# Kernel optimization log

Hardware: AMD Instinct MI355X
Metric: run time of the kernel (lower is better)

The kernel has to match this reference:

```python
import jax, jax.numpy as jnp
import numpy as np
import math

NUM_HEADS = 16
KEY_DIM = 64
MODEL_DIM = 1024
NEG_INF = -1000000000.0


def _get_slopes(n):
    def pow2_slopes(n):
        start = 2 ** (-2 ** (-(math.log2(n) - 3)))
        return [start * start ** i for i in range(n)]
    if math.log2(n).is_integer():
        s = pow2_slopes(n)
    else:
        c = 2 ** math.floor(math.log2(n))
        s = pow2_slopes(c) + pow2_slopes(2 * c)[0::2][: n - c]
    return jnp.asarray(s, dtype=jnp.float32)


def setup_inputs() -> dict:
    key = jax.random.key(0)
    ks = jax.random.split(key, 11)
    B, S, D = 4, 2048, MODEL_DIM
    P = NUM_HEADS * KEY_DIM
    sd = 1.0 / math.sqrt(D)
    return {
        "query": jax.random.normal(ks[0], (B, S, D), jnp.float32),
        "key": jax.random.normal(ks[1], (B, S, D), jnp.float32),
        "value": jax.random.normal(ks[2], (B, S, D), jnp.float32),
        "Wq": jax.random.normal(ks[3], (D, P), jnp.float32) * sd,
        "bq": jnp.zeros((P,), jnp.float32),
        "Wk": jax.random.normal(ks[4], (D, P), jnp.float32) * sd,
        "bk": jnp.zeros((P,), jnp.float32),
        "Wv": jax.random.normal(ks[5], (D, P), jnp.float32) * sd,
        "bv": jnp.zeros((P,), jnp.float32),
        "Wo": jax.random.normal(ks[6], (P, D), jnp.float32) * (1.0 / math.sqrt(P)),
        "bo": jnp.zeros((D,), jnp.float32),
    }


def reference(query, key, value, Wq, bq, Wk, bk, Wv, bv, Wo, bo):
    B, S, _ = query.shape
    H, Kd = NUM_HEADS, KEY_DIM

    def split_heads(x):  # [B,S,H*Kd] -> [B,H,S,Kd]
        return x.reshape(B, S, H, Kd).transpose(0, 2, 1, 3)

    q = split_heads(query @ Wq + bq)
    k = split_heads(key @ Wk + bk)
    v = split_heads(value @ Wv + bv)

    logits = jnp.einsum("bhqd,bhkd->bhqk", q, k) / jnp.sqrt(jnp.float32(Kd))

    i = jnp.arange(S)[:, None]
    j = jnp.arange(S)[None, :]
    causal = jnp.where(i >= j, 0.0, NEG_INF).astype(jnp.float32)  # [S,S]
    rel = (i - j).astype(jnp.float32)  # [S,S]
    slopes = _get_slopes(H)  # [H]
    alibi = slopes[:, None, None] * rel  # [H,S,S]
    logits = logits + causal[None, None, :, :] + alibi[None, :, :, :]

    weights = jax.nn.softmax(logits, axis=-1)
    attn = jnp.einsum("bhqk,bhkd->bhqd", weights, v)
    concat = attn.transpose(0, 2, 1, 3).reshape(B, S, H * Kd)
    return concat @ Wo + bo
```

## Files before the change

### kernel.cpp

```cpp
#include <hip/hip_runtime.h>

#define B_ 4
#define S_ 2048
#define D_ 1024
#define H_ 16
#define KD_ 64
#define P_ 1024
#define M_ (B_*S_)

typedef unsigned short u16;
typedef unsigned int u32;
typedef __attribute__((ext_vector_type(2))) unsigned u32x2;
typedef __attribute__((ext_vector_type(4))) float f32x4;
typedef __attribute__((ext_vector_type(8))) __bf16 bf16x8;

__device__ __forceinline__ u16 f2bf(float f) {
  u32 x = __float_as_uint(f);
  return (u16)((x + 0x7fffu + ((x >> 16) & 1u)) >> 16);
}

__device__ __forceinline__ void gl_lds16(const u16* g, u16* l) {
  __builtin_amdgcn_global_load_lds((__attribute__((address_space(1))) void*)g,
                                   (__attribute__((address_space(3))) void*)l, 16, 0, 0);
}

__device__ __forceinline__ u32 pkbf(float a, float b) {
  return __builtin_amdgcn_perm(__float_as_uint(b) + 0x8000u,
                               __float_as_uint(a) + 0x8000u, 0x07060302u);
}

#if __has_builtin(__builtin_amdgcn_permlane32_swap) && __has_builtin(__builtin_amdgcn_permlane16_swap)
__device__ __forceinline__ void plswap(u32& a, u32& b) {
  u32x2 r32 = __builtin_amdgcn_permlane32_swap(a, b, false, false);
  u32x2 r16 = __builtin_amdgcn_permlane16_swap(r32[0], r32[1], false, false);
  a = r16[0]; b = r16[1];
}
#else
__device__ __forceinline__ void plswap(u32& a, u32& b) {
  const int l = threadIdx.x & 63;
  const int quad = l >> 4, l16 = l & 15;
  int i0 = (((quad & 1) * 32) + l16) * 4;
  int i1 = i0 + 64;
  int a_lo = __builtin_amdgcn_ds_bpermute(i0, (int)a);
  int b_lo = __builtin_amdgcn_ds_bpermute(i0, (int)b);
  int a_hi = __builtin_amdgcn_ds_bpermute(i1, (int)a);
  int b_hi = __builtin_amdgcn_ds_bpermute(i1, (int)b);
  u32 na = (quad < 2) ? (u32)a_lo : (u32)b_lo;
  u32 nb = (quad < 2) ? (u32)a_hi : (u32)b_hi;
  a = na; b = nb;
}
#endif

__global__ void cvt3_kernel(const float* __restrict__ q, const float* __restrict__ k,
                            const float* __restrict__ v,
                            u16* __restrict__ Xq, u16* __restrict__ Xk, u16* __restrict__ Xv) {
  const int z = blockIdx.y;
  const float* in = z == 0 ? q : z == 1 ? k : v;
  u16* out = z == 0 ? Xq : z == 1 ? Xk : Xv;
  int i = blockIdx.x * 256 + threadIdx.x;
  float4 vv = ((const float4*)in)[i];
  ((u32*)out)[i*2+0] = (u32)f2bf(vv.x) | ((u32)f2bf(vv.y) << 16);
  ((u32*)out)[i*2+1] = (u32)f2bf(vv.z) | ((u32)f2bf(vv.w) << 16);
}

__global__ void transpose_cvt4(const float* __restrict__ Wq, const float* __restrict__ Wk,
                               const float* __restrict__ Wv, const float* __restrict__ Wo,
                               u16* __restrict__ WqT, u16* __restrict__ WkT,
                               u16* __restrict__ WvT, u16* __restrict__ WoT) {
  const int z = blockIdx.z;
  const float* in = z == 0 ? Wq : z == 1 ? Wk : z == 2 ? Wv : Wo;
  u16* out = z == 0 ? WqT : z == 1 ? WkT : z == 2 ? WvT : WoT;
  __shared__ float tile[32][33];
  int bx = blockIdx.x * 32, by = blockIdx.y * 32;
  int tx = threadIdx.x, ty = threadIdx.y;
  #pragma unroll
  for (int kk = 0; kk < 4; ++kk)
    tile[ty + kk*8][tx] = in[(by + ty + kk*8) * 1024 + bx + tx];
  __syncthreads();
  #pragma unroll
  for (int kk = 0; kk < 4; ++kk)
    out[(bx + ty + kk*8) * 1024 + by + tx] = f2bf(tile[tx][ty + kk*8]);
}

__global__ __launch_bounds__(256) void gemm_qkv(
    const u16* __restrict__ Xq, const u16* __restrict__ Xk, const u16* __restrict__ Xv,
    const u16* __restrict__ WqT, const u16* __restrict__ WkT, const u16* __restrict__ WvT,
    const float* __restrict__ bq, const float* __restrict__ bk, const float* __restrict__ bv,
    u16* __restrict__ Qb, u16* __restrict__ Kb, u16* __restrict__ Vt)
{
  constexpr int K = 1024, N = 1024, BK = 32;
  const int z = blockIdx.z;
  const u16* A  = z == 0 ? Xq  : z == 1 ? Xk  : Xv;
  const u16* Bt = z == 0 ? WqT : z == 1 ? WkT : WvT;
  const float* bias = z == 0 ? bq : z == 1 ? bk : bv;

  __shared__ alignas(16) u16 As[128*BK];
  __shared__ alignas(16) u16 Bs[128*BK];
  const int tid = threadIdx.x;
  const int w = tid >> 6, l = tid & 63;
  const int quad = l >> 4, l16 = l & 15;
  const int wm = (w >> 1) * 64, wn = (w & 1) * 64;
  const long mBase = (long)blockIdx.x * 128;
  const int  nBase = blockIdx.y * 128;

  f32x4 acc[4][4] = {};
  const int off0 = w*1024 + l*16;

  for (int kb = 0; kb < K/BK; ++kb) {
    __syncthreads();
    #pragma unroll
    for (int p = 0; p < 2; ++p) {
      int off = p*4096 + off0;
      int row = off >> 6;
      int cb  = off & 63;
      const u16* ga = A  + (mBase + row)*K + kb*BK + (cb >> 1);
      const u16* gb = Bt + ((long)(nBase + row))*K + kb*BK + (cb >> 1);
      gl_lds16(ga, (u16*)((char*)As + p*4096 + w*1024));
      gl_lds16(gb, (u16*)((char*)Bs + p*4096 + w*1024));
    }
    __syncthreads();
    bf16x8 af[4], bf[4];
    #pragma unroll
    for (int i = 0; i < 4; ++i) af[i] = *(const bf16x8*)&As[(wm + i*16 + l16)*BK + quad*8];
    #pragma unroll
    for (int j = 0; j < 4; ++j) bf[j] = *(const bf16x8*)&Bs[(wn + j*16 + l16)*BK + quad*8];
    #pragma unroll
    for (int i = 0; i < 4; ++i)
      #pragma unroll
      for (int j = 0; j < 4; ++j)
        acc[i][j] = __builtin_amdgcn_mfma_f32_16x16x32_bf16(af[i], bf[j], acc[i][j], 0, 0, 0);
  }

  if (z < 2) {
    u16* Cout = z == 0 ? Qb : Kb;
    #pragma unroll
    for (int i = 0; i < 4; ++i)
      #pragma unroll
      for (int j = 0; j < 4; ++j)
        #pragma unroll
        for (int r = 0; r < 4; ++r) {
          long row = mBase + wm + i*16 + quad*4 + r;
          int  col = nBase + wn + j*16 + l16;
          Cout[row*N + col] = f2bf(acc[i][j][r] + bias[col]);
        }
  } else {
    #pragma unroll
    for (int i = 0; i < 4; ++i)
      #pragma unroll
      for (int j = 0; j < 4; ++j) {
        int  col  = nBase + wn + j*16 + l16;
        long row0 = mBase + wm + i*16 + quad*4;
        int  bb = (int)(row0 >> 11);
        int  ss = (int)(row0 & 2047);
        float bcol = bias[col];
        float v0 = acc[i][j][0] + bcol, v1 = acc[i][j][1] + bcol;
        float v2 = acc[i][j][2] + bcol, v3 = acc[i][j][3] + bcol;
        uint2 pk;
        pk.x = (u32)f2bf(v0) | ((u32)f2bf(v1) << 16);
        pk.y = (u32)f2bf(v2) | ((u32)f2bf(v3) << 16);
        *(uint2*)&Vt[((long)(bb*16) * 64 + col) * 2048 + ss] = pk;
      }
  }
}

__global__ __launch_bounds__(256) void gemm_out(const u16* __restrict__ A,
                                                const u16* __restrict__ Bt,
                                                const float* __restrict__ bias,
                                                float* __restrict__ Cout)
{
  constexpr int K = 1024, N = 1024, BK = 32;
  __shared__ alignas(16) u16 As[128*BK];
  __shared__ alignas(16) u16 Bs[128*BK];
  const int tid = threadIdx.x;
  const int w = tid >> 6, l = tid & 63;
  const int quad = l >> 4, l16 = l & 15;
  const int wm = (w >> 1) * 64, wn = (w & 1) * 64;
  const long mBase = (long)blockIdx.x * 128;
  const int  nBase = blockIdx.y * 128;

  f32x4 acc[4][4] = {};
  const int off0 = w*1024 + l*16;

  for (int kb = 0; kb < K/BK; ++kb) {
    __syncthreads();
    #pragma unroll
    for (int p = 0; p < 2; ++p) {
      int off = p*4096 + off0;
      int row = off >> 6;
      int cb  = off & 63;
      const u16* ga = A  + (mBase + row)*K + kb*BK + (cb >> 1);
      const u16* gb = Bt + ((long)(nBase + row))*K + kb*BK + (cb >> 1);
      gl_lds16(ga, (u16*)((char*)As + p*4096 + w*1024));
      gl_lds16(gb, (u16*)((char*)Bs + p*4096 + w*1024));
    }
    __syncthreads();
    bf16x8 af[4], bf[4];
    #pragma unroll
    for (int i = 0; i < 4; ++i) af[i] = *(const bf16x8*)&As[(wm + i*16 + l16)*BK + quad*8];
    #pragma unroll
    for (int j = 0; j < 4; ++j) bf[j] = *(const bf16x8*)&Bs[(wn + j*16 + l16)*BK + quad*8];
    #pragma unroll
    for (int i = 0; i < 4; ++i)
      #pragma unroll
      for (int j = 0; j < 4; ++j)
        acc[i][j] = __builtin_amdgcn_mfma_f32_16x16x32_bf16(af[i], bf[j], acc[i][j], 0, 0, 0);
  }

  #pragma unroll
  for (int i = 0; i < 4; ++i)
    #pragma unroll
    for (int j = 0; j < 4; ++j)
      #pragma unroll
      for (int r = 0; r < 4; ++r) {
        long row = mBase + wm + i*16 + quad*4 + r;
        int  col = nBase + wn + j*16 + l16;
        Cout[row*N + col] = acc[i][j][r] + bias[col];
      }
}

__global__ __launch_bounds__(256, 4) void attn_kernel(const u16* __restrict__ Qb,
                                                      const u16* __restrict__ Kb,
                                                      const u16* __restrict__ Vt,
                                                      u16* __restrict__ Ob)
{
  const int n = blockIdx.x;
  const int qt = 15 - (n >> 6);
  const int r6 = n & 63;
  const int b = r6 >> 4, h = r6 & 15;
  const int w = threadIdx.x >> 6;
  const int l = threadIdx.x & 63;
  const int quad = l >> 4, l16 = l & 15;
  const float LOG2E = 1.44269504089f;
  const float slope = exp2f(-0.5f * (float)(h + 1));
  const float c1  = 0.125f * LOG2E;
  const float sl2 = slope * LOG2E;
  const float rs1 = sl2, rs2 = 2.f*sl2, rs3 = 3.f*sl2;

  const int q0 = qt*128 + w*32;
  const u16* Qp = Qb + ((long)(b*S_ + q0))*P_ + h*KD_;
  const u16* Kp = Kb + ((long)(b*S_))*P_ + h*KD_;
  const u16* Vp = Vt + ((long)(b*H_ + h))*KD_*S_;

  bf16x8 qf[2][2];
  #pragma unroll
  for (int i = 0; i < 2; ++i)
    #pragma unroll
    for (int kk = 0; kk < 2; ++kk)
      qf[i][kk] = *(const bf16x8*)&Qp[(long)(i*16 + l16)*P_ + kk*32 + quad*8];

  f32x4 o[2][4] = {};
  float lsum[2] = {0.f, 0.f};

  for (int kt = 0; kt < qt; ++kt) {
    const u16* kts = Kp + (long)(kt*128 + l16)*P_;
    const float kbase = (float)(kt*128);
    #pragma unroll
    for (int ks = 0; ks < 4; ++ks) {
      u32 pw[2][2][2];
      #pragma unroll
      for (int jp = 0; jp < 2; ++jp) {
        const int j = 2*ks + jp;
        const u16* kp = kts + (long)(j*16)*P_;
        bf16x8 kf0 = *(const bf16x8*)(kp + quad*8);
        bf16x8 kf1 = *(const bf16x8*)(kp + 32 + quad*8);
        const float bij = -sl2 * (kbase + (float)(j*16 + quad*4));
        #pragma unroll
        for (int i = 0; i < 2; ++i) {
          f32x4 t = {};
          t = __builtin_amdgcn_mfma_f32_16x16x32_bf16(kf0, qf[i][0], t, 0, 0, 0);
          t = __builtin_amdgcn_mfma_f32_16x16x32_bf16(kf1, qf[i][1], t, 0, 0, 0);
          float p0 = __builtin_amdgcn_exp2f(fmaf(t[0], c1, bij));
          float p1 = __builtin_amdgcn_exp2f(fmaf(t[1], c1, bij) - rs1);
          float p2 = __builtin_amdgcn_exp2f(fmaf(t[2], c1, bij) - rs2);
          float p3 = __builtin_amdgcn_exp2f(fmaf(t[3], c1, bij) - rs3);
          lsum[i] += (p0 + p1) + (p2 + p3);
          pw[i][jp][0] = pkbf(p0, p1);
          pw[i][jp][1] = pkbf(p2, p3);
        }
      }
      bf16x8 pb[2];
      #pragma unroll
      for (int i = 0; i < 2; ++i) {
        u32 fa0 = pw[i][0][0], fb0 = pw[i][1][0];
        u32 fa1 = pw[i][0][1], fb1 = pw[i][1][1];
        plswap(fa0, fb0);
        plswap(fa1, fb1);
        union { u32 u[4]; bf16x8 v; } fu;
        fu.u[0] = fa0; fu.u[1] = fa1; fu.u[2] = fb0; fu.u[3] = fb1;
        pb[i] = fu.v;
      }
      #pragma unroll
      for (int jn = 0; jn < 4; ++jn) {
        bf16x8 vf = *(const bf16x8*)&Vp[(long)(jn*16 + l16)*S_ + kt*128 + ks*32 + quad*8];
        o[0][jn] = __builtin_amdgcn_mfma_f32_16x16x32_bf16(vf, pb[0], o[0][jn], 0, 0, 0);
        o[1][jn] = __builtin_amdgcn_mfma_f32_16x16x32_bf16(vf, pb[1], o[1][jn], 0, 0, 0);
      }
    }
  }

  {
    const int kt = qt;
    const int ksmax = w + 1;
    const u16* kts = Kp + (long)(kt*128 + l16)*P_;
    for (int ks = 0; ks < ksmax; ++ks) {
      u32 pw[2][2][2];
      #pragma unroll
      for (int jp = 0; jp < 2; ++jp) {
        const int j = 2*ks + jp;
        const u16* kp = kts + (long)(j*16)*P_;
        bf16x8 kf0 = *(const bf16x8*)(kp + quad*8);
        bf16x8 kf1 = *(const bf16x8*)(kp + 32 + quad*8);
        const int kl0 = j*16 + quad*4;
        const float bij = -sl2 * (float)(kt*128 + kl0);
        #pragma unroll
        for (int i = 0; i < 2; ++i) {
          const int ql = w*32 + i*16 + l16;
          f32x4 t = {};
          t = __builtin_amdgcn_mfma_f32_16x16x32_bf16(kf0, qf[i][0], t, 0, 0, 0);
          t = __builtin_amdgcn_mfma_f32_16x16x32_bf16(kf1, qf[i][1], t, 0, 0, 0);
          float x0 = fmaf(t[0], c1, bij);
          float x1 = fmaf(t[1], c1, bij) - rs1;
          float x2 = fmaf(t[2], c1, bij) - rs2;
          float x3 = fmaf(t[3], c1, bij) - rs3;
          if (kl0 + 0 > ql) x0 = -1e30f;
          if (kl0 + 1 > ql) x1 = -1e30f;
          if (kl0 + 2 > ql) x2 = -1e30f;
          if (kl0 + 3 > ql) x3 = -1e30f;
          float p0 = __builtin_amdgcn_exp2f(x0);
          float p1 = __builtin_amdgcn_exp2f(x1);
          float p2 = __builtin_amdgcn_exp2f(x2);
          float p3 = __builtin_amdgcn_exp2f(x3);
          lsum[i] += (p0 + p1) + (p2 + p3);
          pw[i][jp][0] = pkbf(p0, p1);
          pw[i][jp][1] = pkbf(p2, p3);
        }
      }
      bf16x8 pb[2];
      #pragma unroll
      for (int i = 0; i < 2; ++i) {
        u32 fa0 = pw[i][0][0], fb0 = pw[i][1][0];
        u32 fa1 = pw[i][0][1], fb1 = pw[i][1][1];
        plswap(fa0, fb0);
        plswap(fa1, fb1);
        union { u32 u[4]; bf16x8 v; } fu;
        fu.u[0] = fa0; fu.u[1] = fa1; fu.u[2] = fb0; fu.u[3] = fb1;
        pb[i] = fu.v;
      }
      #pragma unroll
      for (int jn = 0; jn < 4; ++jn) {
        bf16x8 vf = *(const bf16x8*)&Vp[(long)(jn*16 + l16)*S_ + kt*128 + ks*32 + quad*8];
        o[0][jn] = __builtin_amdgcn_mfma_f32_16x16x32_bf16(vf, pb[0], o[0][jn], 0, 0, 0);
        o[1][jn] = __builtin_amdgcn_mfma_f32_16x16x32_bf16(vf, pb[1], o[1][jn], 0, 0, 0);
      }
    }
  }

  #pragma unroll
  for (int i = 0; i < 2; ++i) {
    lsum[i] += __shfl_xor(lsum[i], 16, 64);
    lsum[i] += __shfl_xor(lsum[i], 32, 64);
    const float inv = 1.0f / lsum[i];
    #pragma unroll
    for (int jn = 0; jn < 4; ++jn) {
      float v0 = o[i][jn][0] * inv, v1 = o[i][jn][1] * inv;
      float v2 = o[i][jn][2] * inv, v3 = o[i][jn][3] * inv;
      uint2 pk;
      pk.x = (u32)f2bf(v0) | ((u32)f2bf(v1) << 16);
      pk.y = (u32)f2bf(v2) | ((u32)f2bf(v3) << 16);
      *(uint2*)&Ob[((long)(b*S_ + q0 + i*16 + l16))*P_ + h*KD_ + jn*16 + quad*4] = pk;
    }
  }
}

extern "C" void kernel_launch(void* const* d_in, const int* in_sizes, int n_in,
                              void* d_out, int out_size, void* d_ws, size_t ws_size,
                              hipStream_t stream) {
  const float* q  = (const float*)d_in[0];
  const float* k  = (const float*)d_in[1];
  const float* v  = (const float*)d_in[2];
  const float* Wq = (const float*)d_in[3];
  const float* bq = (const float*)d_in[4];
  const float* Wk = (const float*)d_in[5];
  const float* bk = (const float*)d_in[6];
  const float* Wv = (const float*)d_in[7];
  const float* bv = (const float*)d_in[8];
  const float* Wo = (const float*)d_in[9];
  const float* bo = (const float*)d_in[10];

  const size_t X_ELEMS = (size_t)M_ * P_;
  const size_t W_ELEMS = (size_t)D_ * P_;
  u16* ws  = (u16*)d_ws;
  u16* Xq  = ws;
  u16* Xk  = Xq  + X_ELEMS;
  u16* Xv  = Xk  + X_ELEMS;
  u16* WqT = Xv  + X_ELEMS;
  u16* WkT = WqT + W_ELEMS;
  u16* WvT = WkT + W_ELEMS;
  u16* WoT = WvT + W_ELEMS;
  u16* Qb  = WoT + W_ELEMS;
  u16* Kb  = Qb  + X_ELEMS;
  u16* Vt  = Kb  + X_ELEMS;
  u16* Attn = Xq;

  cvt3_kernel<<<dim3((unsigned)(X_ELEMS/4/256), 3), 256, 0, stream>>>(q, k, v, Xq, Xk, Xv);

  transpose_cvt4<<<dim3(32, 32, 4), dim3(32, 8), 0, stream>>>(Wq, Wk, Wv, Wo,
                                                              WqT, WkT, WvT, WoT);

  gemm_qkv<<<dim3(M_/128, P_/128, 3), 256, 0, stream>>>(Xq, Xk, Xv, WqT, WkT, WvT,
                                                        bq, bk, bv, Qb, Kb, Vt);

  attn_kernel<<<dim3(1024), 256, 0, stream>>>(Qb, Kb, Vt, Attn);

  gemm_out<<<dim3(M_/128, P_/128), 256, 0, stream>>>(Attn, WoT, bo, (float*)d_out);
}
```

Measured before the change: 401.9 us.

## Pair causal query tiles per block and double-buffer K/V register loads

Each block now processes two query tiles, qt and 15-qt, so every block does the same total work across the causal triangle, and the grid is halved to 512. The full-tile loop is restructured to prefetch the next step's K and V fragments into a second register set while the current step computes. Launch bounds drop to 2 blocks per SM to give room for the extra registers. Together these aim to balance load and hide global-load latency, at the cost of lower occupancy and fewer blocks in flight.

```diff
diff --git a/kernel.cpp b/kernel.cpp
--- a/kernel.cpp
+++ b/kernel.cpp
@@ -218,13 +218,13 @@
       }
 }
 
-__global__ __launch_bounds__(256, 4) void attn_kernel(const u16* __restrict__ Qb,
+__global__ __launch_bounds__(256, 2) void attn_kernel(const u16* __restrict__ Qb,
                                                       const u16* __restrict__ Kb,
                                                       const u16* __restrict__ Vt,
                                                       u16* __restrict__ Ob)
 {
   const int n = blockIdx.x;
-  const int qt = 15 - (n >> 6);
+  const int pairIdx = n >> 6;
   const int r6 = n & 63;
   const int b = r6 >> 4, h = r6 & 15;
   const int w = threadIdx.x >> 6;
@@ -236,138 +236,185 @@
   const float sl2 = slope * LOG2E;
   const float rs1 = sl2, rs2 = 2.f*sl2, rs3 = 3.f*sl2;
 
-  const int q0 = qt*128 + w*32;
-  const u16* Qp = Qb + ((long)(b*S_ + q0))*P_ + h*KD_;
   const u16* Kp = Kb + ((long)(b*S_))*P_ + h*KD_;
   const u16* Vp = Vt + ((long)(b*H_ + h))*KD_*S_;
 
-  bf16x8 qf[2][2];
-  #pragma unroll
-  for (int i = 0; i < 2; ++i)
-    #pragma unroll
-    for (int kk = 0; kk < 2; ++kk)
-      qf[i][kk] = *(const bf16x8*)&Qp[(long)(i*16 + l16)*P_ + kk*32 + quad*8];
-
-  f32x4 o[2][4] = {};
-  float lsum[2] = {0.f, 0.f};
-
-  for (int kt = 0; kt < qt; ++kt) {
-    const u16* kts = Kp + (long)(kt*128 + l16)*P_;
-    const float kbase = (float)(kt*128);
-    #pragma unroll
-    for (int ks = 0; ks < 4; ++ks) {
-      u32 pw[2][2][2];
-      #pragma unroll
-      for (int jp = 0; jp < 2; ++jp) {
-        const int j = 2*ks + jp;
-        const u16* kp = kts + (long)(j*16)*P_;
-        bf16x8 kf0 = *(const bf16x8*)(kp + quad*8);
-        bf16x8 kf1 = *(const bf16x8*)(kp + 32 + quad*8);
-        const float bij = -sl2 * (kbase + (float)(j*16 + quad*4));
+  for (int half = 0; half < 2; ++half) {
+    const int qt = half == 0 ? (15 - pairIdx) : pairIdx;
+    const int q0 = qt*128 + w*32;
+    const u16* Qp = Qb + ((long)(b*S_ + q0))*P_ + h*KD_;
+
+    bf16x8 qf[2][2];
+    #pragma unroll
+    for (int i = 0; i < 2; ++i)
+      #pragma unroll
+      for (int kk = 0; kk < 2; ++kk)
+        qf[i][kk] = *(const bf16x8*)&Qp[(long)(i*16 + l16)*P_ + kk*32 + quad*8];
+
+    f32x4 o[2][4] = {};
+    float lsum[2] = {0.f, 0.f};
+
+    auto issue = [&](int it, bf16x8& k00, bf16x8& k01, bf16x8& k10, bf16x8& k11,
+                     bf16x8& v0, bf16x8& v1, bf16x8& v2, bf16x8& v3) {
+      const int kt = it >> 2, ks = it & 3;
+      const u16* kp = Kp + (long)(kt*128 + l16 + 2*ks*16)*P_;
+      k00 = *(const bf16x8*)(kp + quad*8);
+      k01 = *(const bf16x8*)(kp + 32 + quad*8);
+      k10 = *(const bf16x8*)(kp + 16*P_ + quad*8);
+      k11 = *(const bf16x8*)(kp + 16*P_ + 32 + quad*8);
+      const u16* vp = Vp + (long)l16*S_ + kt*128 + ks*32 + quad*8;
+      v0 = *(const bf16x8*)(vp);
+      v1 = *(const bf16x8*)(vp + 16*S_);
+      v2 = *(const bf16x8*)(vp + 32*S_);
+      v3 = *(const bf16x8*)(vp + 48*S_);
+    };
+    auto compute = [&](int it, const bf16x8& k00, const bf16x8& k01,
+                       const bf16x8& k10, const bf16x8& k11,
+                       const bf16x8& v0, const bf16x8& v1,
+                       const bf16x8& v2, const bf16x8& v3) {
+      const int kt = it >> 2, ks = it & 3;
+      const float kb0 = (float)(kt*128 + 2*ks*16 + quad*4);
+      u32 pw0[2][2], pw1[2][2];
+      {
+        const float bij = -sl2 * kb0;
         #pragma unroll
         for (int i = 0; i < 2; ++i) {
           f32x4 t = {};
-          t = __builtin_amdgcn_mfma_f32_16x16x32_bf16(kf0, qf[i][0], t, 0, 0, 0);
-          t = __builtin_amdgcn_mfma_f32_16x16x32_bf16(kf1, qf[i][1], t, 0, 0, 0);
+          t = __builtin_amdgcn_mfma_f32_16x16x32_bf16(k00, qf[i][0], t, 0, 0, 0);
+          t = __builtin_amdgcn_mfma_f32_16x16x32_bf16(k01, qf[i][1], t, 0, 0, 0);
           float p0 = __builtin_amdgcn_exp2f(fmaf(t[0], c1, bij));
           float p1 = __builtin_amdgcn_exp2f(fmaf(t[1], c1, bij) - rs1);
           float p2 = __builtin_amdgcn_exp2f(fmaf(t[2], c1, bij) - rs2);
           float p3 = __builtin_amdgcn_exp2f(fmaf(t[3], c1, bij) - rs3);
           lsum[i] += (p0 + p1) + (p2 + p3);
-          pw[i][jp][0] = pkbf(p0, p1);
-          pw[i][jp][1] = pkbf(p2, p3);
+          pw0[i][0] = pkbf(p0, p1);
+          pw0[i][1] = pkbf(p2, p3);
+        }
+      }
+      {
+        const float bij = -sl2 * (kb0 + 16.f);
+        #pragma unroll
+        for (int i = 0; i < 2; ++i) {
+          f32x4 t = {};
+          t = __builtin_amdgcn_mfma_f32_16x16x32_bf16(k10, qf[i][0], t, 0, 0, 0);
+          t = __builtin_amdgcn_mfma_f32_16x16x32_bf16(k11, qf[i][1], t, 0, 0, 0);
+          float p0 = __builtin_amdgcn_exp2f(fmaf(t[0], c1, bij));
+          float p1 = __builtin_amdgcn_exp2f(fmaf(t[1], c1, bij) - rs1);
+          float p2 = __builtin_amdgcn_exp2f(fmaf(t[2], c1, bij) - rs2);
+          float p3 = __builtin_amdgcn_exp2f(fmaf(t[3], c1, bij) - rs3);
+          lsum[i] += (p0 + p1) + (p2 + p3);
+          pw1[i][0] = pkbf(p0, p1);
+          pw1[i][1] = pkbf(p2, p3);
         }
       }
       bf16x8 pb[2];
       #pragma unroll
       for (int i = 0; i < 2; ++i) {
-        u32 fa0 = pw[i][0][0], fb0 = pw[i][1][0];
-        u32 fa1 = pw[i][0][1], fb1 = pw[i][1][1];
+        u32 fa0 = pw0[i][0], fb0 = pw1[i][0];
+        u32 fa1 = pw0[i][1], fb1 = pw1[i][1];
         plswap(fa0, fb0);
         plswap(fa1, fb1);
         union { u32 u[4]; bf16x8 v; } fu;
         fu.u[0] = fa0; fu.u[1] = fa1; fu.u[2] = fb0; fu.u[3] = fb1;
         pb[i] = fu.v;
       }
+      o[0][0] = __builtin_amdgcn_mfma_f32_16x16x32_bf16(v0, pb[0], o[0][0], 0, 0, 0);
+      o[1][0] = __builtin_amdgcn_mfma_f32_16x16x32_bf16(v0, pb[1], o[1][0], 0, 0, 0);
+      o[0][1] = __builtin_amdgcn_mfma_f32_16x16x32_bf16(v1, pb[0], o[0][1], 0, 0, 0);
+      o[1][1] = __builtin_amdgcn_mfma_f32_16x16x32_bf16(v1, pb[1], o[1][1], 0, 0, 0);
+      o[0][2] = __builtin_amdgcn_mfma_f32_16x16x32_bf16(v2, pb[0], o[0][2], 0, 0, 0);
+      o[1][2] = __builtin_amdgcn_mfma_f32_16x16x32_bf16(v2, pb[1], o[1][2], 0, 0, 0);
+      o[0][3] = __builtin_amdgcn_mfma_f32_16x16x32_bf16(v3, pb[0], o[0][3], 0, 0, 0);
+      o[1][3] = __builtin_amdgcn_mfma_f32_16x16x32_bf16(v3, pb[1], o[1][3], 0, 0, 0);
+    };
+
+    const int nit = qt * 4;
+    if (nit > 0) {
+      bf16x8 ak00, ak01, ak10, ak11, av0, av1, av2, av3;
+      bf16x8 bk00, bk01, bk10, bk11, bv0, bv1, bv2, bv3;
+      issue(0, ak00, ak01, ak10, ak11, av0, av1, av2, av3);
+      int it = 0;
+      while (true) {
+        if (it + 1 < nit) issue(it + 1, bk00, bk01, bk10, bk11, bv0, bv1, bv2, bv3);
+        compute(it, ak00, ak01, ak10, ak11, av0, av1, av2, av3);
+        ++it; if (it == nit) break;
+        if (it + 1 < nit) issue(it + 1, ak00, ak01, ak10, ak11, av0, av1, av2, av3);
+        compute(it, bk00, bk01, bk10, bk11, bv0, bv1, bv2, bv3);
+        ++it; if (it == nit) break;
+      }
+    }
+
+    {
+      const int kt = qt;
+      const int ksmax = w + 1;
+      const u16* kts = Kp + (long)(kt*128 + l16)*P_;
+      for (int ks = 0; ks < ksmax; ++ks) {
+        u32 pw[2][2][2];
+        #pragma unroll
+        for (int jp = 0; jp < 2; ++jp) {
+          const int j = 2*ks + jp;
+          const u16* kp = kts + (long)(j*16)*P_;
+          bf16x8 kf0 = *(const bf16x8*)(kp + quad*8);
+          bf16x8 kf1 = *(const bf16x8*)(kp + 32 + quad*8);
+          const int kl0 = j*16 + quad*4;
+          const float bij = -sl2 * (float)(kt*128 + kl0);
+          #pragma unroll
+          for (int i = 0; i < 2; ++i) {
+            const int ql = w*32 + i*16 + l16;
+            f32x4 t = {};
+            t = __builtin_amdgcn_mfma_f32_16x16x32_bf16(kf0, qf[i][0], t, 0, 0, 0);
+            t = __builtin_amdgcn_mfma_f32_16x16x32_bf16(kf1, qf[i][1], t, 0, 0, 0);
+            float x0 = fmaf(t[0], c1, bij);
+            float x1 = fmaf(t[1], c1, bij) - rs1;
+            float x2 = fmaf(t[2], c1, bij) - rs2;
+            float x3 = fmaf(t[3], c1, bij) - rs3;
+            if (kl0 + 0 > ql) x0 = -1e30f;
+            if (kl0 + 1 > ql) x1 = -1e30f;
+            if (kl0 + 2 > ql) x2 = -1e30f;
+            if (kl0 + 3 > ql) x3 = -1e30f;
+            float p0 = __builtin_amdgcn_exp2f(x0);
+            float p1 = __builtin_amdgcn_exp2f(x1);
+            float p2 = __builtin_amdgcn_exp2f(x2);
+            float p3 = __builtin_amdgcn_exp2f(x3);
+            lsum[i] += (p0 + p1) + (p2 + p3);
+            pw[i][jp][0] = pkbf(p0, p1);
+            pw[i][jp][1] = pkbf(p2, p3);
+          }
+        }
+        bf16x8 pb[2];
+        #pragma unroll
+        for (int i = 0; i < 2; ++i) {
+          u32 fa0 = pw[i][0][0], fb0 = pw[i][1][0];
+          u32 fa1 = pw[i][0][1], fb1 = pw[i][1][1];
+          plswap(fa0, fb0);
+          plswap(fa1, fb1);
+          union { u32 u[4]; bf16x8 v; } fu;
+          fu.u[0] = fa0; fu.u[1] = fa1; fu.u[2] = fb0; fu.u[3] = fb1;
+          pb[i] = fu.v;
+        }
+        #pragma unroll
+        for (int jn = 0; jn < 4; ++jn) {
+          bf16x8 vf = *(const bf16x8*)&Vp[(long)(jn*16 + l16)*S_ + kt*128 + ks*32 + quad*8];
+          o[0][jn] = __builtin_amdgcn_mfma_f32_16x16x32_bf16(vf, pb[0], o[0][jn], 0, 0, 0);
+          o[1][jn] = __builtin_amdgcn_mfma_f32_16x16x32_bf16(vf, pb[1], o[1][jn], 0, 0, 0);
+        }
+      }
+    }
+
+    #pragma unroll
+    for (int i = 0; i < 2; ++i) {
+      lsum[i] += __shfl_xor(lsum[i], 16, 64);
+      lsum[i] += __shfl_xor(lsum[i], 32, 64);
+      const float inv = 1.0f / lsum[i];
       #pragma unroll
       for (int jn = 0; jn < 4; ++jn) {
-        bf16x8 vf = *(const bf16x8*)&Vp[(long)(jn*16 + l16)*S_ + kt*128 + ks*32 + quad*8];
-        o[0][jn] = __builtin_amdgcn_mfma_f32_16x16x32_bf16(vf, pb[0], o[0][jn], 0, 0, 0);
-        o[1][jn] = __builtin_amdgcn_mfma_f32_16x16x32_bf16(vf, pb[1], o[1][jn], 0, 0, 0);
-      }
-    }
-  }
-
-  {
-    const int kt = qt;
-    const int ksmax = w + 1;
-    const u16* kts = Kp + (long)(kt*128 + l16)*P_;
-    for (int ks = 0; ks < ksmax; ++ks) {
-      u32 pw[2][2][2];
-      #pragma unroll
-      for (int jp = 0; jp < 2; ++jp) {
-        const int j = 2*ks + jp;
-        const u16* kp = kts + (long)(j*16)*P_;
-        bf16x8 kf0 = *(const bf16x8*)(kp + quad*8);
-        bf16x8 kf1 = *(const bf16x8*)(kp + 32 + quad*8);
-        const int kl0 = j*16 + quad*4;
-        const float bij = -sl2 * (float)(kt*128 + kl0);
-        #pragma unroll
-        for (int i = 0; i < 2; ++i) {
-          const int ql = w*32 + i*16 + l16;
-          f32x4 t = {};
-          t = __builtin_amdgcn_mfma_f32_16x16x32_bf16(kf0, qf[i][0], t, 0, 0, 0);
-          t = __builtin_amdgcn_mfma_f32_16x16x32_bf16(kf1, qf[i][1], t, 0, 0, 0);
-          float x0 = fmaf(t[0], c1, bij);
-          float x1 = fmaf(t[1], c1, bij) - rs1;
-          float x2 = fmaf(t[2], c1, bij) - rs2;
-          float x3 = fmaf(t[3], c1, bij) - rs3;
-          if (kl0 + 0 > ql) x0 = -1e30f;
-          if (kl0 + 1 > ql) x1 = -1e30f;
-          if (kl0 + 2 > ql) x2 = -1e30f;
-          if (kl0 + 3 > ql) x3 = -1e30f;
-          float p0 = __builtin_amdgcn_exp2f(x0);
-          float p1 = __builtin_amdgcn_exp2f(x1);
-          float p2 = __builtin_amdgcn_exp2f(x2);
-          float p3 = __builtin_amdgcn_exp2f(x3);
-          lsum[i] += (p0 + p1) + (p2 + p3);
-          pw[i][jp][0] = pkbf(p0, p1);
-          pw[i][jp][1] = pkbf(p2, p3);
-        }
-      }
-      bf16x8 pb[2];
-      #pragma unroll
-      for (int i = 0; i < 2; ++i) {
-        u32 fa0 = pw[i][0][0], fb0 = pw[i][1][0];
-        u32 fa1 = pw[i][0][1], fb1 = pw[i][1][1];
-        plswap(fa0, fb0);
-        plswap(fa1, fb1);
-        union { u32 u[4]; bf16x8 v; } fu;
-        fu.u[0] = fa0; fu.u[1] = fa1; fu.u[2] = fb0; fu.u[3] = fb1;
-        pb[i] = fu.v;
-      }
-      #pragma unroll
-      for (int jn = 0; jn < 4; ++jn) {
-        bf16x8 vf = *(const bf16x8*)&Vp[(long)(jn*16 + l16)*S_ + kt*128 + ks*32 + quad*8];
-        o[0][jn] = __builtin_amdgcn_mfma_f32_16x16x32_bf16(vf, pb[0], o[0][jn], 0, 0, 0);
-        o[1][jn] = __builtin_amdgcn_mfma_f32_16x16x32_bf16(vf, pb[1], o[1][jn], 0, 0, 0);
-      }
-    }
-  }
-
-  #pragma unroll
-  for (int i = 0; i < 2; ++i) {
-    lsum[i] += __shfl_xor(lsum[i], 16, 64);
-    lsum[i] += __shfl_xor(lsum[i], 32, 64);
-    const float inv = 1.0f / lsum[i];
-    #pragma unroll
-    for (int jn = 0; jn < 4; ++jn) {
-      float v0 = o[i][jn][0] * inv, v1 = o[i][jn][1] * inv;
-      float v2 = o[i][jn][2] * inv, v3 = o[i][jn][3] * inv;
-      uint2 pk;
-      pk.x = (u32)f2bf(v0) | ((u32)f2bf(v1) << 16);
-      pk.y = (u32)f2bf(v2) | ((u32)f2bf(v3) << 16);
-      *(uint2*)&Ob[((long)(b*S_ + q0 + i*16 + l16))*P_ + h*KD_ + jn*16 + quad*4] = pk;
+        float v0 = o[i][jn][0] * inv, v1 = o[i][jn][1] * inv;
+        float v2 = o[i][jn][2] * inv, v3 = o[i][jn][3] * inv;
+        uint2 pk;
+        pk.x = (u32)f2bf(v0) | ((u32)f2bf(v1) << 16);
+        pk.y = (u32)f2bf(v2) | ((u32)f2bf(v3) << 16);
+        *(uint2*)&Ob[((long)(b*S_ + q0 + i*16 + l16))*P_ + h*KD_ + jn*16 + quad*4] = pk;
+      }
     }
   }
 }
@@ -410,7 +457,7 @@
   gemm_qkv<<<dim3(M_/128, P_/128, 3), 256, 0, stream>>>(Xq, Xk, Xv, WqT, WkT, WvT,
                                                         bq, bk, bv, Qb, Kb, Vt);
 
-  attn_kernel<<<dim3(1024), 256, 0, stream>>>(Qb, Kb, Vt, Attn);
+  attn_kernel<<<dim3(512), 256, 0, stream>>>(Qb, Kb, Vt, Attn);
 
   gemm_out<<<dim3(M_/128, P_/128), 256, 0, stream>>>(Attn, WoT, bo, (float*)d_out);
 }
```

Measured after the change: 381.2 us. 5.2% less time.
